# Performance work log

Measured on AMD Instinct MI355X. Metric: run time of the kernel, lower is better.

The kernel has to match this reference:

```python
import jax, jax.numpy as jnp
import numpy as np

RANK = 24          # init: rank
WHITEN = True      # init: whiten
NS_ITERS = 5       # Newton-Schulz iterations for inverse matrix square root
EPS = 1e-5         # covariance jitter


def _ns_inv_sqrt(C, iters=NS_ITERS):
    # Newton-Schulz iteration computing C^{-1/2} for SPD C: (B, N, N).
    N = C.shape[-1]
    I = jnp.eye(N, dtype=C.dtype)
    normC = jnp.sqrt(jnp.sum(C * C, axis=(-2, -1), keepdims=True))  # Frobenius norm
    Y = C / normC
    Z = jnp.broadcast_to(I, C.shape)
    for _ in range(iters):
        T = 0.5 * (3.0 * I - Z @ Y)
        Y = Y @ T
        Z = T @ Z
    return Z / jnp.sqrt(normC)  # Z -> norm^{1/2} * C^{-1/2}


def _whiten(X):
    # X: (B, n, N) -> X @ Cov(X)^{-1/2}
    n = X.shape[-2]
    N = X.shape[-1]
    C = jnp.einsum('bnd,bne->bde', X, X) / n + EPS * jnp.eye(N, dtype=X.dtype)
    return X @ _ns_inv_sqrt(C)


def _procrustes_rotation(M):
    # M = S^T T (B, d, d); orthogonal R = U Vh minimizing ||S R - T||_F (Kabsch).
    U, _, Vh = jnp.linalg.svd(M, full_matrices=False)
    return U @ Vh


def _align(source, target, rank=RANK, whiten=WHITEN):
    S = _whiten(source) if whiten else source
    T = _whiten(target) if whiten else target
    N = S.shape[-1]
    if N <= 32:
        # full Procrustes
        R = _procrustes_rotation(jnp.einsum('bnd,bne->bde', S, T))
        aligned = S @ R
    else:
        # project to rank-r joint subspace, align there, lift back with
        # identity on the orthogonal complement: R = Q Rr Q^T + (I - Q Q^T)
        X = jnp.concatenate([S, T], axis=1)                 # (B, 2n, N)
        _, _, Vh = jnp.linalg.svd(X, full_matrices=False)    # Vh: (B, N', N)
        Q = jnp.swapaxes(Vh[:, :rank, :], -2, -1)            # (B, N, r)
        Sp = S @ Q                                           # (B, n, r)
        Tp = T @ Q
        Rr = _procrustes_rotation(jnp.einsum('bnr,bns->brs', Sp, Tp))  # (B, r, r) small SVD
        # aligned = S @ (Q Rr Q^T + I - Q Q^T) = S + Sp (Rr - I) Q^T
        aligned = S + Sp @ (Rr - jnp.eye(rank, dtype=S.dtype)) @ jnp.swapaxes(Q, -2, -1)
    return aligned


def setup_inputs() -> dict:
    key = jax.random.key(0)
    k1, k2 = jax.random.split(key)
    source = jax.random.normal(k1, (64, 512, 384), dtype=jnp.float32)
    target = jax.random.normal(k2, (64, 512, 384), dtype=jnp.float32)
    return {"source": source, "target": target}


def reference(source, target):
    aligned = _align(source, target)
    # diagnostic: mean cosine similarity between aligned and target rows
    cos = jnp.sum(aligned * target, axis=-1) / (
        jnp.linalg.norm(aligned, axis=-1) * jnp.linalg.norm(target, axis=-1) + 1e-8)
    cos_after = jnp.mean(cos)
    return aligned, cos_after
```

## Files before the change

### kernel.cpp

```cpp
#include <hip/hip_runtime.h>
#include <math.h>

static constexpr int BATCH = 64;
static constexpr int NR  = 512;
static constexpr int ND  = 384;
static constexpr int RK  = 24;
static constexpr int NSI = 5;
static constexpr int POLAR_ITERS = 36;
static constexpr int PNB = 32;
static constexpr long SZC = (long)BATCH * ND * ND;
static constexpr int SSTR = BATCH * RK;

#define MODE_PLAIN 0
#define MODE_COV   1
#define MODE_NST   2
#define MODE_SCALE 3
#define MODE_ACC   4

typedef _Float16 half8 __attribute__((ext_vector_type(8)));
typedef _Float16 half4 __attribute__((ext_vector_type(4)));
typedef float floatx4 __attribute__((ext_vector_type(4)));

template<int TA>
__global__ __launch_bounds__(256)
void gemm_kernel(const float* __restrict__ Ag, const float* __restrict__ Bg,
                 float* __restrict__ Cg, int M, int N, int K,
                 long sA, long sB, long sC, int lda, int ldb, int ldc,
                 int mode, const float* __restrict__ scale)
{
    const int batch = blockIdx.y;
    const int tilesN = N >> 7;
    const int tx = blockIdx.x % tilesN;
    const int ty = blockIdx.x / tilesN;
    const int n0 = tx * 128, m0 = ty * 128;
    const float* A = Ag + (long)batch * sA;
    const float* Bm = Bg + (long)batch * sB;
    float* C = Cg + (long)batch * sC;

    __shared__ _Float16 Ah[128][40], Al[128][40];
    __shared__ _Float16 Bh[128][40], Bl[128][40];

    const int tid = threadIdx.x;
    const int wave = tid >> 6, lane = tid & 63;
    const int wm0 = (wave >> 1) * 64, wn0 = (wave & 1) * 64;
    const int fm = lane & 15;
    const int fq = lane >> 4;

    floatx4 acc[4][4];
#pragma unroll
    for (int i = 0; i < 4; i++)
#pragma unroll
        for (int j = 0; j < 4; j++) acc[i][j] = (floatx4){0.f, 0.f, 0.f, 0.f};

    for (int k0 = 0; k0 < K; k0 += 32) {
        if (TA == 0) {
#pragma unroll
            for (int q = 0; q < 4; q++) {
                int idx = tid + q * 256;
                int row = idx >> 3, kq = (idx & 7) * 4;
                float4 v = *(const float4*)&A[(long)(m0 + row) * lda + k0 + kq];
                _Float16 h0 = (_Float16)v.x; _Float16 l0 = (_Float16)(v.x - (float)h0);
                _Float16 h1 = (_Float16)v.y; _Float16 l1 = (_Float16)(v.y - (float)h1);
                _Float16 h2 = (_Float16)v.z; _Float16 l2 = (_Float16)(v.z - (float)h2);
                _Float16 h3 = (_Float16)v.w; _Float16 l3 = (_Float16)(v.w - (float)h3);
                half4 hv, lv;
                hv[0] = h0; hv[1] = h1; hv[2] = h2; hv[3] = h3;
                lv[0] = l0; lv[1] = l1; lv[2] = l2; lv[3] = l3;
                *(half4*)&Ah[row][kq] = hv;
                *(half4*)&Al[row][kq] = lv;
            }
        } else {
            int m = tid & 127, kb = (tid >> 7) * 16;
            _Float16 hbuf[16], lbuf[16];
#pragma unroll
            for (int i = 0; i < 16; i++) {
                float v = A[(long)(k0 + kb + i) * lda + m0 + m];
                _Float16 hh = (_Float16)v;
                hbuf[i] = hh; lbuf[i] = (_Float16)(v - (float)hh);
            }
#pragma unroll
            for (int i = 0; i < 16; i += 4) {
                half4 hv, lv;
                hv[0] = hbuf[i]; hv[1] = hbuf[i + 1]; hv[2] = hbuf[i + 2]; hv[3] = hbuf[i + 3];
                lv[0] = lbuf[i]; lv[1] = lbuf[i + 1]; lv[2] = lbuf[i + 2]; lv[3] = lbuf[i + 3];
                *(half4*)&Ah[m][kb + i] = hv;
                *(half4*)&Al[m][kb + i] = lv;
            }
        }
        {
            int n = tid & 127, kb = (tid >> 7) * 16;
            _Float16 hbuf[16], lbuf[16];
#pragma unroll
            for (int i = 0; i < 16; i++) {
                float v = Bm[(long)(k0 + kb + i) * ldb + n0 + n];
                _Float16 hh = (_Float16)v;
                hbuf[i] = hh; lbuf[i] = (_Float16)(v - (float)hh);
            }
#pragma unroll
            for (int i = 0; i < 16; i += 4) {
                half4 hv, lv;
                hv[0] = hbuf[i]; hv[1] = hbuf[i + 1]; hv[2] = hbuf[i + 2]; hv[3] = hbuf[i + 3];
                lv[0] = lbuf[i]; lv[1] = lbuf[i + 1]; lv[2] = lbuf[i + 2]; lv[3] = lbuf[i + 3];
                *(half4*)&Bh[n][kb + i] = hv;
                *(half4*)&Bl[n][kb + i] = lv;
            }
        }
        __syncthreads();

        half8 ah[4], alv[4], bh[4], blv[4];
#pragma unroll
        for (int mt = 0; mt < 4; mt++) {
            ah[mt]  = *(const half8*)&Ah[wm0 + mt * 16 + fm][fq * 8];
            alv[mt] = *(const half8*)&Al[wm0 + mt * 16 + fm][fq * 8];
        }
#pragma unroll
        for (int nt = 0; nt < 4; nt++) {
            bh[nt]  = *(const half8*)&Bh[wn0 + nt * 16 + fm][fq * 8];
            blv[nt] = *(const half8*)&Bl[wn0 + nt * 16 + fm][fq * 8];
        }
#pragma unroll
        for (int mt = 0; mt < 4; mt++) {
#pragma unroll
            for (int nt = 0; nt < 4; nt++) {
                floatx4 a = acc[mt][nt];
                a = __builtin_amdgcn_mfma_f32_16x16x32_f16(alv[mt], bh[nt], a, 0, 0, 0);
                a = __builtin_amdgcn_mfma_f32_16x16x32_f16(ah[mt], blv[nt], a, 0, 0, 0);
                a = __builtin_amdgcn_mfma_f32_16x16x32_f16(ah[mt], bh[nt], a, 0, 0, 0);
                acc[mt][nt] = a;
            }
        }
        __syncthreads();
    }

    float scl = 1.f;
    if (mode == MODE_SCALE) scl = 1.0f / sqrtf(scale[batch]);

#pragma unroll
    for (int mt = 0; mt < 4; mt++) {
#pragma unroll
        for (int nt = 0; nt < 4; nt++) {
            int gn = n0 + wn0 + nt * 16 + fm;
#pragma unroll
            for (int r = 0; r < 4; r++) {
                int gm = m0 + wm0 + mt * 16 + fq * 4 + r;
                float v = acc[mt][nt][r];
                float* cp = C + (long)gm * ldc + gn;
                if (mode == MODE_COV)      v = v * (1.0f / 512.0f) + ((gm == gn) ? 1e-5f : 0.f);
                else if (mode == MODE_NST) v = ((gm == gn) ? 1.5f : 0.f) - 0.5f * v;
                else if (mode == MODE_SCALE) v *= scl;
                else if (mode == MODE_ACC) v += *cp;
                *cp = v;
            }
        }
    }
}

__global__ __launch_bounds__(256)
void frob_kernel(const float* __restrict__ Cm, float* __restrict__ nrm)
{
    int b = blockIdx.x;
    const float* p = Cm + (long)b * ND * ND;
    float s = 0.f;
    for (int i = threadIdx.x; i < ND * ND; i += 256) { float v = p[i]; s += v * v; }
    __shared__ float red[256];
    red[threadIdx.x] = s; __syncthreads();
    for (int off = 128; off > 0; off >>= 1) {
        if (threadIdx.x < off) red[threadIdx.x] += red[threadIdx.x + off];
        __syncthreads();
    }
    if (threadIdx.x == 0) nrm[b] = sqrtf(red[0]);
}

__global__ __launch_bounds__(256)
void init_kernel(float* __restrict__ Y, float* __restrict__ Z, const float* __restrict__ nrm)
{
    const int total = BATCH * ND * ND;
    for (int idx = blockIdx.x * 256 + threadIdx.x; idx < total; idx += gridDim.x * 256) {
        int b = idx / (ND * ND);
        int rem = idx - b * (ND * ND);
        int r = rem / ND, c = rem - r * ND;
        Y[idx] = Y[idx] / nrm[b];
        Z[idx] = (r == c) ? 1.f : 0.f;
    }
}

__device__ __forceinline__ float bred768(float v, float* red12, int t)
{
#pragma unroll
    for (int off = 32; off > 0; off >>= 1) v += __shfl_down(v, off);
    if ((t & 63) == 0) red12[t >> 6] = v;
    __syncthreads();
    float r = 0.f;
#pragma unroll
    for (int i = 0; i < 12; i++) r += red12[i];
    __syncthreads();
    return r;
}

__global__ __launch_bounds__(768)
void tridiag_panel(float* __restrict__ Gall, float* __restrict__ dA,
                   float* __restrict__ eA, float* __restrict__ tauA,
                   float* __restrict__ Wgall, int k0)
{
    int b = blockIdx.x;
    float* A = Gall + (long)b * ND * ND;
    float* Wg = Wgall + (long)b * (PNB * ND);
    float* d = dA + b * ND; float* e = eA + b * ND; float* tau = tauA + b * ND;
    const int t = threadIdx.x;
    const int h = (t >= ND) ? 1 : 0;
    const int c = t - h * ND;
    const int g = t % 96;
    const int s = t / 96;
    __shared__ float Ul[PNB][ND];
    __shared__ float Wl[PNB][ND];
    __shared__ float u_s[ND];
    __shared__ float pp4s[8][392];
    __shared__ float al[PNB], be[PNB];
    __shared__ float red12[12];
    __shared__ float s_tau;

    const int jcnt = min(PNB, ND - 2 - k0);

    for (int j = 0; j < jcnt; j++) {
        const int k = k0 + j;
        const int m = ND - 1 - k;
        float x = 0.f;
        if (!h && c < m) {
            const int kc = (k + 1) + c;
            x = A[(long)k * ND + kc];
#pragma unroll 4
            for (int l = 0; l < j; l++) {
                x -= Ul[l][k] * Wl[l][kc] + Wl[l][k] * Ul[l][kc];
            }
            u_s[c] = x;
        }
        float sigma = bred768(x * x, red12, t);
        if (t == 0) {
            float v0 = u_s[0];
            float normx = sqrtf(sigma);
            float alpha = (v0 >= 0.f) ? -normx : normx;
            float denom = sigma - alpha * v0;
            float tk = (denom > 1e-30f) ? 1.f / denom : 0.f;
            s_tau = tk;
            float diag = A[(long)k * ND + k];
            for (int l = 0; l < j; l++) diag -= 2.f * Ul[l][k] * Wl[l][k];
            e[k] = alpha; tau[k] = tk; d[k] = diag;
            u_s[0] = v0 - alpha;
        }
        __syncthreads();
        const float tk = s_tau;

        const int kk4 = (k + 1) & ~3;
        const int off = (k + 1) - kk4;
        const int ncol4 = 96 - (kk4 >> 2);
        if (g < ncol4) {
            const int ri0 = (m * s) >> 3;
            const int ri1 = (m * (s + 1)) >> 3;
            const float* base = A + (long)(k + 1) * ND + kk4 + 4 * g;
            floatx4 p4 = (floatx4){0.f, 0.f, 0.f, 0.f};
            int i = ri0;
            for (; i + 8 <= ri1; i += 8) {
                floatx4 a0 = *(const floatx4*)&base[(long)(i    ) * ND];
                floatx4 a1 = *(const floatx4*)&base[(long)(i + 1) * ND];
                floatx4 a2 = *(const floatx4*)&base[(long)(i + 2) * ND];
                floatx4 a3 = *(const floatx4*)&base[(long)(i + 3) * ND];
                floatx4 a4 = *(const floatx4*)&base[(long)(i + 4) * ND];
                floatx4 a5 = *(const floatx4*)&base[(long)(i + 5) * ND];
                floatx4 a6 = *(const floatx4*)&base[(long)(i + 6) * ND];
                floatx4 a7 = *(const floatx4*)&base[(long)(i + 7) * ND];
                p4 += a0 * u_s[i]     + a1 * u_s[i + 1] + a2 * u_s[i + 2] + a3 * u_s[i + 3]
                    + a4 * u_s[i + 4] + a5 * u_s[i + 5] + a6 * u_s[i + 6] + a7 * u_s[i + 7];
            }
            for (; i < ri1; i++) {
                floatx4 a0 = *(const floatx4*)&base[(long)i * ND];
                p4 += a0 * u_s[i];
            }
            *(floatx4*)&pp4s[s][4 * g] = p4;
        }
        {
            int wv = t >> 6, ln = t & 63;
            for (int l = wv; l < j; l += 12) {
                float sa = 0.f, sb = 0.f;
                const float* wrow = &Wl[l][k + 1];
                const float* urow = &Ul[l][k + 1];
                for (int i = ln; i < m; i += 64) { sa += wrow[i] * u_s[i]; sb += urow[i] * u_s[i]; }
#pragma unroll
                for (int off2 = 32; off2 > 0; off2 >>= 1) {
                    sa += __shfl_down(sa, off2); sb += __shfl_down(sb, off2);
                }
                if (ln == 0) { al[l] = sa; be[l] = sb; }
            }
        }
        __syncthreads();
        float contrib = 0.f, pc = 0.f;
        if (!h && c < m) {
            int ca = c + off;
            pc = pp4s[0][ca] + pp4s[1][ca] + pp4s[2][ca] + pp4s[3][ca]
               + pp4s[4][ca] + pp4s[5][ca] + pp4s[6][ca] + pp4s[7][ca];
            const int kc = (k + 1) + c;
#pragma unroll 4
            for (int l = 0; l < j; l++) {
                pc -= al[l] * Ul[l][kc] + be[l] * Wl[l][kc];
            }
            pc *= tk;
            contrib = u_s[c] * pc;
        }
        float dotup = bred768(contrib, red12, t);
        float sc = 0.5f * tk * dotup;
        if (!h && c < m) {
            const int kc = (k + 1) + c;
            float uv = u_s[c];
            float w = pc - sc * uv;
            Wl[j][kc] = w;
            Ul[j][kc] = uv;
            Wg[j * ND + kc] = w;
            A[(long)k * ND + kc] = uv;
        }
        __syncthreads();
    }
    if (k0 + PNB >= ND - 2 && t == 0) {
        float d0 = A[(long)(ND - 2) * ND + (ND - 2)];
        float e0 = A[(long)(ND - 2) * ND + (ND - 1)];
        float d1 = A[(long)(ND - 1) * ND + (ND - 1)];
        for (int l = 0; l < jcnt; l++) {
            float u0 = A[(long)(k0 + l) * ND + (ND - 2)];
            float u1 = A[(long)(k0 + l) * ND + (ND - 1)];
            float w0 = Wg[l * ND + (ND - 2)];
            float w1 = Wg[l * ND + (ND - 1)];
            d0 -= 2.f * u0 * w0;
            e0 -= u0 * w1 + w0 * u1;
            d1 -= 2.f * u1 * w1;
        }
        d[ND - 2] = d0; d[ND - 1] = d1; e[ND - 2] = e0;
        e[ND - 1] = 0.f; tau[ND - 2] = 0.f; tau[ND - 1] = 0.f;
    }
}

__global__ __launch_bounds__(256)
void syr2k_update(float* __restrict__ Gall, const float* __restrict__ Wgall, int k0)
{
    const int k1 = k0 + PNB;
    const int tiles = (ND - k1) >> 5;
    int b = blockIdx.y;
    int ti = blockIdx.x / tiles, tj = blockIdx.x % tiles;
    int i0 = k1 + ti * 32, c0 = k1 + tj * 32;
    float* A = Gall + (long)b * ND * ND;
    const float* Wg = Wgall + (long)b * (PNB * ND);

    __shared__ float Us[PNB][36], Ws[PNB][36], Uc[PNB][36], Wc[PNB][36];
    int t = threadIdx.x;
    for (int q = t; q < PNB * 8; q += 256) {
        int l = q >> 3, c4 = (q & 7) * 4;
        *(float4*)&Us[l][c4] = *(const float4*)&A[(long)(k0 + l) * ND + i0 + c4];
        *(float4*)&Ws[l][c4] = *(const float4*)&Wg[l * ND + i0 + c4];
        *(float4*)&Uc[l][c4] = *(const float4*)&A[(long)(k0 + l) * ND + c0 + c4];
        *(float4*)&Wc[l][c4] = *(const float4*)&Wg[l * ND + c0 + c4];
    }
    __syncthreads();
    int tr = t >> 4, tc = t & 15;
    float acc00 = 0.f, acc01 = 0.f, acc10 = 0.f, acc11 = 0.f;
#pragma unroll 4
    for (int l = 0; l < PNB; l++) {
        float ua0 = Us[l][tr * 2], ua1 = Us[l][tr * 2 + 1];
        float wa0 = Ws[l][tr * 2], wa1 = Ws[l][tr * 2 + 1];
        float ub0 = Uc[l][tc * 2], ub1 = Uc[l][tc * 2 + 1];
        float wb0 = Wc[l][tc * 2], wb1 = Wc[l][tc * 2 + 1];
        acc00 += ua0 * wb0 + wa0 * ub0;
        acc01 += ua0 * wb1 + wa0 * ub1;
        acc10 += ua1 * wb0 + wa1 * ub0;
        acc11 += ua1 * wb1 + wa1 * ub1;
    }
    {
        float* r0 = &A[(long)(i0 + tr * 2) * ND + c0 + tc * 2];
        float* r1 = r0 + ND;
        float2 o0 = *(const float2*)r0, o1 = *(const float2*)r1;
        o0.x -= acc00; o0.y -= acc01;
        o1.x -= acc10; o1.y -= acc11;
        *(float2*)r0 = o0; *(float2*)r1 = o1;
    }
}

__global__ __launch_bounds__(64)
void eigvals_kernel(const float* __restrict__ dA, const float* __restrict__ eA,
                    float* __restrict__ lamA)
{
    int b = blockIdx.x, t = threadIdx.x;
    __shared__ float2 de[ND];
    __shared__ float d_s[ND], ea[ND], red[64];
    for (int i = t; i < ND; i += 64) {
        float dv = dA[b * ND + i];
        float ev = eA[b * ND + i];
        float ep = (i > 0) ? eA[b * ND + i - 1] : 0.f;
        d_s[i] = dv; ea[i] = fabsf(ev);
        de[i] = make_float2(dv, ep * ep + 1e-38f);
    }
    __syncthreads();
    float lo = 1e30f, hi = -1e30f;
    for (int i = t; i < ND; i += 64) {
        float r = ea[i] + ((i > 0) ? ea[i - 1] : 0.f);
        lo = fminf(lo, d_s[i] - r); hi = fmaxf(hi, d_s[i] + r);
    }
    red[t] = lo; __syncthreads();
    for (int off = 32; off > 0; off >>= 1) {
        if (t < off) red[t] = fminf(red[t], red[t + off]);
        __syncthreads();
    }
    lo = red[0]; __syncthreads();
    red[t] = hi; __syncthreads();
    for (int off = 32; off > 0; off >>= 1) {
        if (t < off) red[t] = fmaxf(red[t], red[t + off]);
        __syncthreads();
    }
    hi = red[0];
    if (t < RK) {
        int idx = ND - 1 - t;
        float a = lo, c = hi;
        for (int it = 0; it < 42; it++) {
            float mid = 0.5f * (a + c);
            int cnt = 0;
            float qinv = 0.f;
            for (int i = 0; i < ND; i += 8) {
                float2 v0 = de[i    ], v1 = de[i + 1], v2 = de[i + 2], v3 = de[i + 3];
                float2 v4 = de[i + 4], v5 = de[i + 5], v6 = de[i + 6], v7 = de[i + 7];
                float q;
                q = (v0.x - mid) - v0.y * qinv; cnt += (q < 0.f); qinv = __builtin_amdgcn_rcpf(q);
                q = (v1.x - mid) - v1.y * qinv; cnt += (q < 0.f); qinv = __builtin_amdgcn_rcpf(q);
                q = (v2.x - mid) - v2.y * qinv; cnt += (q < 0.f); qinv = __builtin_amdgcn_rcpf(q);
                q = (v3.x - mid) - v3.y * qinv; cnt += (q < 0.f); qinv = __builtin_amdgcn_rcpf(q);
                q = (v4.x - mid) - v4.y * qinv; cnt += (q < 0.f); qinv = __builtin_amdgcn_rcpf(q);
                q = (v5.x - mid) - v5.y * qinv; cnt += (q < 0.f); qinv = __builtin_amdgcn_rcpf(q);
                q = (v6.x - mid) - v6.y * qinv; cnt += (q < 0.f); qinv = __builtin_amdgcn_rcpf(q);
                q = (v7.x - mid) - v7.y * qinv; cnt += (q < 0.f); qinv = __builtin_amdgcn_rcpf(q);
            }
            if (cnt > idx) c = mid; else a = mid;
        }
        lamA[b * RK + t] = 0.5f * (a + c);
    }
}

__global__ __launch_bounds__(64)
void invit_kernel(const float* __restrict__ dA, const float* __restrict__ eA,
                  const float* __restrict__ lamA, float* __restrict__ scr)
{
    int b = blockIdx.x, t = threadIdx.x;
    __shared__ float d[ND], e[ND];
    __shared__ float ua[ND][RK], ub[ND][RK], uc[ND][RK];
    __shared__ float y[ND][RK];
    for (int i = t; i < ND; i += 64) { d[i] = dA[b * ND + i]; e[i] = eA[b * ND + i]; }
    __syncthreads();
    if (t >= RK) return;
    const int s = b * RK + t;
    float* yout = scr + 5L * ND * SSTR;
    const float lam = lamA[s];

    for (int pass = 0; pass < 2; pass++) {
        if (pass == 0) {
            for (int i = 0; i < ND; i++) {
                unsigned h = ((unsigned)i * 1103515245u) ^ ((unsigned)s * 747796405u);
                h *= 2654435769u; h ^= h >> 16;
                y[i][t] = ((float)(h & 0xFFFFu) * (1.f / 65536.f)) - 0.5f;
            }
        }
        float ai = d[0] - lam;
        float bc = e[0];
        float ycur = y[0][t];
        for (int i = 0; i < ND - 1; i++) {
            float sub = e[i];
            float dn = d[i + 1] - lam;
            float en = (i + 1 < ND - 1) ? e[i + 1] : 0.f;
            float ynext = y[i + 1][t];
            if (fabsf(ai) >= fabsf(sub)) {
                float aa = (ai == 0.f) ? 1e-20f : ai;
                float mlt = sub / aa;
                ua[i][t] = aa; ub[i][t] = bc; uc[i][t] = 0.f;
                y[i][t] = ycur;
                ycur = ynext - mlt * ycur;
                ai = dn - mlt * bc;
                bc = en;
            } else {
                float mlt = ai / sub;
                ua[i][t] = sub; ub[i][t] = dn; uc[i][t] = en;
                y[i][t] = ynext;
                ycur = ycur - mlt * ynext;
                ai = bc - mlt * dn;
                bc = -mlt * en;
            }
        }
        float uaN = (ai == 0.f) ? 1e-20f : ai;
        float x1 = ycur / uaN;
        y[ND - 1][t] = x1;
        float x2 = x1;
        {
            float xm = (y[ND - 2][t] - ub[ND - 2][t] * x1) / ua[ND - 2][t];
            y[ND - 2][t] = xm; x2 = x1; x1 = xm;
        }
        for (int i = ND - 3; i >= 0; i--) {
            float xi = (y[i][t] - ub[i][t] * x1 - uc[i][t] * x2) / ua[i][t];
            y[i][t] = xi; x2 = x1; x1 = xi;
        }
        float nn = 0.f;
        for (int i = 0; i < ND; i++) { float v = y[i][t]; nn += v * v; }
        float inv = (nn > 0.f) ? 1.f / sqrtf(nn) : 0.f;
        for (int i = 0; i < ND; i++) y[i][t] *= inv;
    }
    for (int i = 0; i < ND; i++) yout[(long)i * SSTR + s] = y[i][t];
}

__global__ __launch_bounds__(384)
void orthbt_kernel(const float* __restrict__ xx, const float* __restrict__ Gall,
                   const float* __restrict__ tauA, float* __restrict__ Qout)
{
    int b = blockIdx.x, t = threadIdx.x;
    __shared__ float Y[ND][RK + 1];
    __shared__ float red[ND];
    __shared__ float dts[RK];
    __shared__ float tls[ND];

    for (int j = 0; j < RK; j++) Y[t][j] = xx[(long)t * SSTR + b * RK + j];
    tls[t] = tauA[b * ND + t];
    __syncthreads();

    const int mcol = t % RK;
    const int msl  = t / RK;
    const int r0m  = msl * 24;
    for (int j = 0; j < RK; j++) {
        float pp = 0.f;
        for (int i = 0; i < 24; i++) {
            pp += Y[r0m + i][j] * Y[r0m + i][mcol];
        }
        red[mcol * 16 + msl] = pp;
        __syncthreads();
        if (t < RK) {
            float ssum = 0.f;
            for (int q = 0; q < 16; q++) ssum += red[t * 16 + q];
            dts[t] = ssum;
        }
        __syncthreads();
        float nv = dts[j];
        float inv = (nv > 1e-30f) ? (1.f / sqrtf(nv)) : 0.f;
        if (mcol > j) {
            float coef = dts[mcol] * inv * inv;
            for (int i = 0; i < 24; i++) Y[r0m + i][mcol] -= coef * Y[r0m + i][j];
        } else if (mcol == j) {
            for (int i = 0; i < 24; i++) Y[r0m + i][j] *= inv;
        }
        __syncthreads();
    }

    const int wv = t >> 6, ln = t & 63;
    float yr[4][6];
#pragma unroll
    for (int cc = 0; cc < 4; cc++)
#pragma unroll
        for (int q = 0; q < 6; q++)
            yr[cc][q] = Y[ln + 64 * q][4 * wv + cc];
    __syncthreads();

    const float* A = Gall + (long)b * ND * ND;
    float un[6];
    {
        const int k = ND - 3;
#pragma unroll
        for (int q = 0; q < 6; q++) un[q] = A[(long)k * ND + ln + 64 * q];
    }
    for (int k = ND - 3; k >= 0; k--) {
        float cu[6];
#pragma unroll
        for (int q = 0; q < 6; q++) {
            int r = ln + 64 * q;
            cu[q] = (r > k) ? un[q] : 0.f;
        }
        if (k > 0) {
#pragma unroll
            for (int q = 0; q < 6; q++) un[q] = A[(long)(k - 1) * ND + ln + 64 * q];
        }
        const float tk = tls[k];
#pragma unroll
        for (int cc = 0; cc < 4; cc++) {
            float p = 0.f;
#pragma unroll
            for (int q = 0; q < 6; q++) p += cu[q] * yr[cc][q];
#pragma unroll
            for (int off = 32; off > 0; off >>= 1) p += __shfl_xor(p, off);
            float sv = tk * p;
#pragma unroll
            for (int q = 0; q < 6; q++) yr[cc][q] -= sv * cu[q];
        }
    }

#pragma unroll
    for (int cc = 0; cc < 4; cc++)
#pragma unroll
        for (int q = 0; q < 6; q++)
            Y[ln + 64 * q][4 * wv + cc] = yr[cc][q];
    __syncthreads();
    for (int l = t; l < ND * RK; l += 384) {
        int i = l / RK, j = l - i * RK;
        Qout[(long)b * ND * RK + l] = Y[i][j];
    }
}

__global__ __launch_bounds__(256)
void proj_kernel(const float* __restrict__ Xw, const float* __restrict__ Qall,
                 float* __restrict__ P)
{
    int b = blockIdx.y;
    int r0 = blockIdx.x * 256;
    __shared__ float Qs[ND][RK + 1];
    const float* Q = Qall + (long)b * ND * RK;
    for (int l = threadIdx.x; l < ND * RK; l += 256) {
        int i = l / RK, j = l - i * RK;
        Qs[i][j] = Q[l];
    }
    __syncthreads();
    int r = r0 + threadIdx.x;
    const float* X = Xw + (long)b * NR * ND + (long)r * ND;
    float acc[RK];
#pragma unroll
    for (int j = 0; j < RK; j++) acc[j] = 0.f;
    for (int k = 0; k < ND; k++) {
        float xv = X[k];
#pragma unroll
        for (int j = 0; j < RK; j++) acc[j] += xv * Qs[k][j];
    }
    float* Pr = P + (long)b * NR * RK + (long)r * RK;
#pragma unroll
    for (int j = 0; j < RK; j++) Pr[j] = acc[j];
}

__global__ __launch_bounds__(256)
void polar_kernel(const float* __restrict__ Sp, const float* __restrict__ Tp,
                  float* __restrict__ RmI)
{
    int b = blockIdx.x, t = threadIdx.x;
    __shared__ float Sb[128][RK + 1], Tb[128][RK + 1];
    __shared__ float Xm[RK][RK + 1], Bm[RK][RK + 1], Mm[RK][RK + 1];
    __shared__ float red[256];

    float accM[3] = {0.f, 0.f, 0.f};
    for (int c = 0; c < 4; c++) {
        for (int l = t; l < 128 * RK; l += 256) {
            int row = l / RK, colj = l - row * RK;
            Sb[row][colj] = Sp[(long)b * NR * RK + (long)(c * 128 + row) * RK + colj];
            Tb[row][colj] = Tp[(long)b * NR * RK + (long)(c * 128 + row) * RK + colj];
        }
        __syncthreads();
        for (int q = 0; q < 3; q++) {
            int e = t + q * 256;
            if (e < RK * RK) {
                int r = e / RK, s2 = e - r * RK;
                float a = 0.f;
                for (int n = 0; n < 128; n++) a += Sb[n][r] * Tb[n][s2];
                accM[q] += a;
            }
        }
        __syncthreads();
    }
    float ss = 0.f;
    for (int q = 0; q < 3; q++) {
        int e = t + q * 256;
        if (e < RK * RK) {
            int r = e / RK, s2 = e - r * RK;
            Mm[r][s2] = accM[q];
            ss += accM[q] * accM[q];
        }
    }
    red[t] = ss; __syncthreads();
    for (int off = 128; off > 0; off >>= 1) {
        if (t < off) red[t] += red[t + off];
        __syncthreads();
    }
    float fro = sqrtf(red[0]);
    float inv = (fro > 1e-30f) ? 1.f / fro : 0.f;
    for (int q = 0; q < 3; q++) {
        int e = t + q * 256;
        if (e < RK * RK) { int r = e / RK, s2 = e - r * RK; Xm[r][s2] = Mm[r][s2] * inv; }
    }
    __syncthreads();
    for (int it = 0; it < POLAR_ITERS; it++) {
        for (int q = 0; q < 3; q++) {
            int e = t + q * 256;
            if (e < RK * RK) {
                int r = e / RK, s2 = e - r * RK;
                float a = 0.f;
                for (int k = 0; k < RK; k++) a += Xm[k][r] * Xm[k][s2];
                Bm[r][s2] = a;
            }
        }
        __syncthreads();
        for (int q = 0; q < 3; q++) {
            int e = t + q * 256;
            if (e < RK * RK) {
                int r = e / RK, s2 = e - r * RK;
                float a = 0.f;
                for (int k = 0; k < RK; k++) a += Xm[r][k] * Bm[k][s2];
                Mm[r][s2] = 1.5f * Xm[r][s2] - 0.5f * a;
            }
        }
        __syncthreads();
        for (int q = 0; q < 3; q++) {
            int e = t + q * 256;
            if (e < RK * RK) { int r = e / RK, s2 = e - r * RK; Xm[r][s2] = Mm[r][s2]; }
        }
        __syncthreads();
    }
    for (int q = 0; q < 3; q++) {
        int e = t + q * 256;
        if (e < RK * RK) {
            int r = e / RK, s2 = e - r * RK;
            RmI[(long)b * RK * RK + e] = Xm[r][s2] - ((r == s2) ? 1.f : 0.f);
        }
    }
}

__global__ __launch_bounds__(256)
void align_kernel(const float* __restrict__ Sw, const float* __restrict__ Sp,
                  const float* __restrict__ RmI, const float* __restrict__ Qall,
                  float* __restrict__ out)
{
    int b = blockIdx.y;
    int r0 = blockIdx.x * 64;
    int t = threadIdx.x;
    __shared__ float Qs[ND][RK + 1];
    __shared__ float Rm[RK][RK + 1];
    __shared__ float Ss[64][RK + 1];
    __shared__ float W[64][RK + 1];

    for (int l = t; l < ND * RK; l += 256) {
        int i = l / RK, j = l - i * RK;
        Qs[i][j] = Qall[(long)b * ND * RK + l];
    }
    for (int l = t; l < RK * RK; l += 256) {
        int i = l / RK, j = l - i * RK;
        Rm[i][j] = RmI[(long)b * RK * RK + l];
    }
    for (int l = t; l < 64 * RK; l += 256) {
        int i = l / RK, j = l - i * RK;
        Ss[i][j] = Sp[(long)b * NR * RK + (long)(r0 + i) * RK + j];
    }
    __syncthreads();
    for (int l = t; l < 64 * RK; l += 256) {
        int r = l / RK, j = l - r * RK;
        float a = 0.f;
        for (int k = 0; k < RK; k++) a += Ss[r][k] * Rm[k][j];
        W[r][j] = a;
    }
    __syncthreads();
    for (int r = 0; r < 64; r++) {
        for (int c = t; c < ND; c += 256) {
            float a = Sw[(long)b * NR * ND + (long)(r0 + r) * ND + c];
            float s2 = 0.f;
#pragma unroll
            for (int j = 0; j < RK; j++) s2 += W[r][j] * Qs[c][j];
            out[(long)b * NR * ND + (long)(r0 + r) * ND + c] = a + s2;
        }
    }
}

__global__ __launch_bounds__(256)
void cos_kernel(const float* __restrict__ out, const float* __restrict__ tgt,
                float* __restrict__ acc)
{
    int row = blockIdx.x * 4 + (threadIdx.x >> 6);
    int lane = threadIdx.x & 63;
    const float* a = out + (long)row * ND;
    const float* tg = tgt + (long)row * ND;
    float sd = 0.f, sa = 0.f, st = 0.f;
    for (int i = lane; i < ND; i += 64) {
        float av = a[i], tv = tg[i];
        sd += av * tv; sa += av * av; st += tv * tv;
    }
#pragma unroll
    for (int off = 32; off > 0; off >>= 1) {
        sd += __shfl_down(sd, off); sa += __shfl_down(sa, off); st += __shfl_down(st, off);
    }
    __shared__ float part[4];
    if (lane == 0) part[threadIdx.x >> 6] = sd / (sqrtf(sa) * sqrtf(st) + 1e-8f);
    __syncthreads();
    if (threadIdx.x == 0) atomicAdd(acc, part[0] + part[1] + part[2] + part[3]);
}

__global__ void finalize_kernel(const float* __restrict__ acc, float* __restrict__ out)
{
    out[0] = acc[0] / 32768.0f;
}

static inline void launch_gemm(int TA, const float* A, const float* Bm, float* C,
                               int M, int N, int K, long sA, long sB, long sC,
                               int lda, int ldb, int ldc, int mode,
                               const float* scale, hipStream_t stream)
{
    dim3 grid((M / 128) * (N / 128), BATCH);
    if (TA)
        gemm_kernel<1><<<grid, dim3(256), 0, stream>>>(A, Bm, C, M, N, K, sA, sB, sC, lda, ldb, ldc, mode, scale);
    else
        gemm_kernel<0><<<grid, dim3(256), 0, stream>>>(A, Bm, C, M, N, K, sA, sB, sC, lda, ldb, ldc, mode, scale);
}

extern "C" void kernel_launch(void* const* d_in, const int* in_sizes, int n_in,
                              void* d_out, int out_size, void* d_ws, size_t ws_size,
                              hipStream_t stream)
{
    const float* src = (const float*)d_in[0];
    const float* tgt = (const float*)d_in[1];
    float* out = (float*)d_out;
    float* ws = (float*)d_ws;

    float* A0 = ws;
    float* A1 = ws + 1 * SZC;
    float* A2 = ws + 2 * SZC;
    float* A3 = ws + 3 * SZC;
    float* A4 = ws + 4 * SZC;
    float* S5 = ws + 5 * SZC;
    float* nrm_s = S5;
    float* nrm_t = S5 + 64;
    float* dd = S5 + 128;
    float* ee = dd + BATCH * ND;
    float* tt = ee + BATCH * ND;
    float* lam = tt + BATCH * ND;
    float* accp = lam + BATCH * RK;

    float* Tm = out;
    float* SW = A0;
    float* TW = A0 + (long)BATCH * NR * ND;
    float* G  = A3;
    float* scr = A4;
    float* Qp  = A4 + 6L * ND * SSTR;
    float* Spp = Qp + (long)BATCH * ND * RK;
    float* Tpp = Spp + (long)BATCH * NR * RK;
    float* Rp  = Tpp + (long)BATCH * NR * RK;
    float* Wg  = Rp + (long)BATCH * RK * RK;
    float* yarr = scr + 5L * ND * SSTR;

    const long sXin = (long)NR * ND;
    const long sSq  = (long)ND * ND;

    launch_gemm(1, src, src, A0, ND, ND, NR, sXin, sXin, sSq, ND, ND, ND, MODE_COV, nullptr, stream);
    frob_kernel<<<BATCH, 256, 0, stream>>>(A0, nrm_s);
    init_kernel<<<dim3(4096), 256, 0, stream>>>(A0, A2, nrm_s);
    {
        float* Y = A0; float* Yo = A1; float* Z = A2; float* Zo = A3;
        for (int it = 0; it < NSI; it++) {
            launch_gemm(0, Z, Y, Tm, ND, ND, ND, sSq, sSq, sSq, ND, ND, ND, MODE_NST, nullptr, stream);
            launch_gemm(0, Y, Tm, Yo, ND, ND, ND, sSq, sSq, sSq, ND, ND, ND, MODE_PLAIN, nullptr, stream);
            launch_gemm(0, Tm, Z, Zo, ND, ND, ND, sSq, sSq, sSq, ND, ND, ND, MODE_PLAIN, nullptr, stream);
            float* tmp = Y; Y = Yo; Yo = tmp;
            tmp = Z; Z = Zo; Zo = tmp;
        }
    }
    launch_gemm(1, tgt, tgt, A0, ND, ND, NR, sXin, sXin, sSq, ND, ND, ND, MODE_COV, nullptr, stream);
    frob_kernel<<<BATCH, 256, 0, stream>>>(A0, nrm_t);
    init_kernel<<<dim3(4096), 256, 0, stream>>>(A0, A2, nrm_t);
    {
        float* Y = A0; float* Yo = A1; float* Z = A2; float* Zo = A4;
        for (int it = 0; it < NSI; it++) {
            launch_gemm(0, Z, Y, Tm, ND, ND, ND, sSq, sSq, sSq, ND, ND, ND, MODE_NST, nullptr, stream);
            launch_gemm(0, Y, Tm, Yo, ND, ND, ND, sSq, sSq, sSq, ND, ND, ND, MODE_PLAIN, nullptr, stream);
            launch_gemm(0, Tm, Z, Zo, ND, ND, ND, sSq, sSq, sSq, ND, ND, ND, MODE_PLAIN, nullptr, stream);
            float* tmp = Y; Y = Yo; Yo = tmp;
            tmp = Z; Z = Zo; Zo = tmp;
        }
    }
    launch_gemm(0, src, A3, SW, NR, ND, ND, sXin, sSq, sXin, ND, ND, ND, MODE_SCALE, nrm_s, stream);
    launch_gemm(0, tgt, A4, TW, NR, ND, ND, sXin, sSq, sXin, ND, ND, ND, MODE_SCALE, nrm_t, stream);
    launch_gemm(1, SW, SW, G, ND, ND, NR, sXin, sXin, sSq, ND, ND, ND, MODE_PLAIN, nullptr, stream);
    launch_gemm(1, TW, TW, G, ND, ND, NR, sXin, sXin, sSq, ND, ND, ND, MODE_ACC, nullptr, stream);
    for (int p = 0; p < ND / PNB; p++) {
        tridiag_panel<<<BATCH, 768, 0, stream>>>(G, dd, ee, tt, Wg, p * PNB);
        int k1 = (p + 1) * PNB;
        if (k1 < ND - 2) {
            int tiles = (ND - k1) >> 5;
            syr2k_update<<<dim3(tiles * tiles, BATCH), 256, 0, stream>>>(G, Wg, p * PNB);
        }
    }
    eigvals_kernel<<<BATCH, 64, 0, stream>>>(dd, ee, lam);
    invit_kernel<<<BATCH, 64, 0, stream>>>(dd, ee, lam, scr);
    orthbt_kernel<<<BATCH, 384, 0, stream>>>(yarr, G, tt, Qp);
    proj_kernel<<<dim3(2, BATCH), 256, 0, stream>>>(SW, Qp, Spp);
    proj_kernel<<<dim3(2, BATCH), 256, 0, stream>>>(TW, Qp, Tpp);
    polar_kernel<<<BATCH, 256, 0, stream>>>(Spp, Tpp, Rp);
    align_kernel<<<dim3(8, BATCH), 256, 0, stream>>>(SW, Spp, Rp, Qp, out);
    hipMemsetAsync((void*)accp, 0, 4, stream);
    cos_kernel<<<dim3(8192), 256, 0, stream>>>(out, tgt, accp);
    finalize_kernel<<<1, 1, 0, stream>>>(accp, out + (long)BATCH * NR * ND);
    (void)in_sizes; (void)n_in; (void)out_size; (void)ws_size;
}
```

Baseline: 5.774 ms.

## Exploit symmetry in Newton-Schulz and covariance GEMMs and fuse the T construction

The Newton-Schulz iteration is reformulated so that every iterate is a symmetric polynomial in the normalized covariance. The separate T = 1.5I - 0.5ZY GEMM output mode is replaced by applying that affine map on the fly while the A/B operand tiles are loaded (tmask). A symmetric mode computes only the upper-triangular 128x128 tiles and mirrors them with transposed stores, and it is applied to the covariance, Gram and NS GEMMs. The aim is to cut MFMA work and tile count by roughly a third. In exchange the mirrored writes are uncoalesced, and the reordered iteration relies on commutativity, which holds only up to floating-point error.

```diff
diff --git a/kernel.cpp b/kernel.cpp
--- a/kernel.cpp
+++ b/kernel.cpp
@@ -5,7 +5,6 @@
 static constexpr int NR  = 512;
 static constexpr int ND  = 384;
 static constexpr int RK  = 24;
-static constexpr int NSI = 5;
 static constexpr int POLAR_ITERS = 36;
 static constexpr int PNB = 32;
 static constexpr long SZC = (long)BATCH * ND * ND;
@@ -13,7 +12,6 @@
 
 #define MODE_PLAIN 0
 #define MODE_COV   1
-#define MODE_NST   2
 #define MODE_SCALE 3
 #define MODE_ACC   4
 
@@ -26,13 +24,21 @@
 void gemm_kernel(const float* __restrict__ Ag, const float* __restrict__ Bg,
                  float* __restrict__ Cg, int M, int N, int K,
                  long sA, long sB, long sC, int lda, int ldb, int ldc,
-                 int mode, const float* __restrict__ scale)
+                 int mode, const float* __restrict__ scale, int sym, int tmask)
 {
     const int batch = blockIdx.y;
     const int tilesN = N >> 7;
-    const int tx = blockIdx.x % tilesN;
-    const int ty = blockIdx.x / tilesN;
-    const int n0 = tx * 128, m0 = ty * 128;
+    int ti, tj;
+    if (sym) {
+        int idx = blockIdx.x;
+        ti = 0; int rem = tilesN;
+        while (idx >= rem) { idx -= rem; ti++; rem--; }
+        tj = ti + idx;
+    } else {
+        tj = blockIdx.x % tilesN;
+        ti = blockIdx.x / tilesN;
+    }
+    const int n0 = tj * 128, m0 = ti * 128;
     const float* A = Ag + (long)batch * sA;
     const float* Bm = Bg + (long)batch * sB;
     float* C = Cg + (long)batch * sC;
@@ -59,6 +65,13 @@
                 int idx = tid + q * 256;
                 int row = idx >> 3, kq = (idx & 7) * 4;
                 float4 v = *(const float4*)&A[(long)(m0 + row) * lda + k0 + kq];
+                if (tmask & 1) {
+                    int gr = m0 + row, gc = k0 + kq;
+                    v.x = ((gr == gc    ) ? 1.5f : 0.f) - 0.5f * v.x;
+                    v.y = ((gr == gc + 1) ? 1.5f : 0.f) - 0.5f * v.y;
+                    v.z = ((gr == gc + 2) ? 1.5f : 0.f) - 0.5f * v.z;
+                    v.w = ((gr == gc + 3) ? 1.5f : 0.f) - 0.5f * v.w;
+                }
                 _Float16 h0 = (_Float16)v.x; _Float16 l0 = (_Float16)(v.x - (float)h0);
                 _Float16 h1 = (_Float16)v.y; _Float16 l1 = (_Float16)(v.y - (float)h1);
                 _Float16 h2 = (_Float16)v.z; _Float16 l2 = (_Float16)(v.z - (float)h2);
@@ -93,6 +106,7 @@
 #pragma unroll
             for (int i = 0; i < 16; i++) {
                 float v = Bm[(long)(k0 + kb + i) * ldb + n0 + n];
+                if (tmask & 2) v = (((k0 + kb + i) == (n0 + n)) ? 1.5f : 0.f) - 0.5f * v;
                 _Float16 hh = (_Float16)v;
                 hbuf[i] = hh; lbuf[i] = (_Float16)(v - (float)hh);
             }
@@ -143,13 +157,19 @@
 #pragma unroll
             for (int r = 0; r < 4; r++) {
                 int gm = m0 + wm0 + mt * 16 + fq * 4 + r;
-                float v = acc[mt][nt][r];
+                float a = acc[mt][nt][r];
                 float* cp = C + (long)gm * ldc + gn;
-                if (mode == MODE_COV)      v = v * (1.0f / 512.0f) + ((gm == gn) ? 1e-5f : 0.f);
-                else if (mode == MODE_NST) v = ((gm == gn) ? 1.5f : 0.f) - 0.5f * v;
-                else if (mode == MODE_SCALE) v *= scl;
-                else if (mode == MODE_ACC) v += *cp;
+                float v = a;
+                if (mode == MODE_COV)      v = a * (1.0f / 512.0f) + ((gm == gn) ? 1e-5f : 0.f);
+                else if (mode == MODE_SCALE) v = a * scl;
+                else if (mode == MODE_ACC) v = a + *cp;
                 *cp = v;
+                if (sym && ti != tj) {
+                    float* cq = C + (long)gn * ldc + gm;
+                    float vq = v;
+                    if (mode == MODE_ACC) vq = a + *cq;
+                    *cq = vq;
+                }
             }
         }
     }
@@ -172,15 +192,16 @@
 }
 
 __global__ __launch_bounds__(256)
-void init_kernel(float* __restrict__ Y, float* __restrict__ Z, const float* __restrict__ nrm)
+void initns_kernel(float* __restrict__ Mb, float* __restrict__ Z, const float* __restrict__ nrm)
 {
     const int total = BATCH * ND * ND;
     for (int idx = blockIdx.x * 256 + threadIdx.x; idx < total; idx += gridDim.x * 256) {
         int b = idx / (ND * ND);
         int rem = idx - b * (ND * ND);
         int r = rem / ND, c = rem - r * ND;
-        Y[idx] = Y[idx] / nrm[b];
-        Z[idx] = (r == c) ? 1.f : 0.f;
+        float v = Mb[idx] / nrm[b];
+        Mb[idx] = v;
+        Z[idx] = ((r == c) ? 1.5f : 0.f) - 0.5f * v;
     }
 }
 
@@ -788,13 +809,16 @@
 static inline void launch_gemm(int TA, const float* A, const float* Bm, float* C,
                                int M, int N, int K, long sA, long sB, long sC,
                                int lda, int ldb, int ldc, int mode,
-                               const float* scale, hipStream_t stream)
-{
-    dim3 grid((M / 128) * (N / 128), BATCH);
+                               const float* scale, int sym, int tmask, hipStream_t stream)
+{
+    int tiles;
+    if (sym) { int tn = N >> 7; tiles = tn * (tn + 1) / 2; }
+    else tiles = (M / 128) * (N / 128);
+    dim3 grid(tiles, BATCH);
     if (TA)
-        gemm_kernel<1><<<grid, dim3(256), 0, stream>>>(A, Bm, C, M, N, K, sA, sB, sC, lda, ldb, ldc, mode, scale);
+        gemm_kernel<1><<<grid, dim3(256), 0, stream>>>(A, Bm, C, M, N, K, sA, sB, sC, lda, ldb, ldc, mode, scale, sym, tmask);
     else
-        gemm_kernel<0><<<grid, dim3(256), 0, stream>>>(A, Bm, C, M, N, K, sA, sB, sC, lda, ldb, ldc, mode, scale);
+        gemm_kernel<0><<<grid, dim3(256), 0, stream>>>(A, Bm, C, M, N, K, sA, sB, sC, lda, ldb, ldc, mode, scale, sym, tmask);
 }
 
 extern "C" void kernel_launch(void* const* d_in, const int* in_sizes, int n_in,
@@ -823,6 +847,7 @@
     float* Tm = out;
     float* SW = A0;
     float* TW = A0 + (long)BATCH * NR * ND;
+    float* B4 = TW;
     float* G  = A3;
     float* scr = A4;
     float* Qp  = A4 + 6L * ND * SSTR;
@@ -835,36 +860,42 @@
     const long sXin = (long)NR * ND;
     const long sSq  = (long)ND * ND;
 
-    launch_gemm(1, src, src, A0, ND, ND, NR, sXin, sXin, sSq, ND, ND, ND, MODE_COV, nullptr, stream);
-    frob_kernel<<<BATCH, 256, 0, stream>>>(A0, nrm_s);
-    init_kernel<<<dim3(4096), 256, 0, stream>>>(A0, A2, nrm_s);
-    {
-        float* Y = A0; float* Yo = A1; float* Z = A2; float* Zo = A3;
-        for (int it = 0; it < NSI; it++) {
-            launch_gemm(0, Z, Y, Tm, ND, ND, ND, sSq, sSq, sSq, ND, ND, ND, MODE_NST, nullptr, stream);
-            launch_gemm(0, Y, Tm, Yo, ND, ND, ND, sSq, sSq, sSq, ND, ND, ND, MODE_PLAIN, nullptr, stream);
-            launch_gemm(0, Tm, Z, Zo, ND, ND, ND, sSq, sSq, sSq, ND, ND, ND, MODE_PLAIN, nullptr, stream);
-            float* tmp = Y; Y = Yo; Yo = tmp;
-            tmp = Z; Z = Zo; Zo = tmp;
-        }
-    }
-    launch_gemm(1, tgt, tgt, A0, ND, ND, NR, sXin, sXin, sSq, ND, ND, ND, MODE_COV, nullptr, stream);
-    frob_kernel<<<BATCH, 256, 0, stream>>>(A0, nrm_t);
-    init_kernel<<<dim3(4096), 256, 0, stream>>>(A0, A2, nrm_t);
-    {
-        float* Y = A0; float* Yo = A1; float* Z = A2; float* Zo = A4;
-        for (int it = 0; it < NSI; it++) {
-            launch_gemm(0, Z, Y, Tm, ND, ND, ND, sSq, sSq, sSq, ND, ND, ND, MODE_NST, nullptr, stream);
-            launch_gemm(0, Y, Tm, Yo, ND, ND, ND, sSq, sSq, sSq, ND, ND, ND, MODE_PLAIN, nullptr, stream);
-            launch_gemm(0, Tm, Z, Zo, ND, ND, ND, sSq, sSq, sSq, ND, ND, ND, MODE_PLAIN, nullptr, stream);
-            float* tmp = Y; Y = Yo; Yo = tmp;
-            tmp = Z; Z = Zo; Zo = tmp;
-        }
-    }
-    launch_gemm(0, src, A3, SW, NR, ND, ND, sXin, sSq, sXin, ND, ND, ND, MODE_SCALE, nrm_s, stream);
-    launch_gemm(0, tgt, A4, TW, NR, ND, ND, sXin, sSq, sXin, ND, ND, ND, MODE_SCALE, nrm_t, stream);
-    launch_gemm(1, SW, SW, G, ND, ND, NR, sXin, sXin, sSq, ND, ND, ND, MODE_PLAIN, nullptr, stream);
-    launch_gemm(1, TW, TW, G, ND, ND, NR, sXin, sXin, sSq, ND, ND, ND, MODE_ACC, nullptr, stream);
+    launch_gemm(1, src, src, A3, ND, ND, NR, sXin, sXin, sSq, ND, ND, ND, MODE_COV, nullptr, 1, 0, stream);
+    frob_kernel<<<BATCH, 256, 0, stream>>>(A3, nrm_s);
+    initns_kernel<<<dim3(2048), 256, 0, stream>>>(A3, A4, nrm_s);
+    launch_gemm(0, A3, A3, Tm, ND, ND, ND, sSq, sSq, sSq, ND, ND, ND, MODE_PLAIN, nullptr, 1, 3, stream);
+    launch_gemm(0, A3, Tm, A0, ND, ND, ND, sSq, sSq, sSq, ND, ND, ND, MODE_PLAIN, nullptr, 1, 0, stream);
+    launch_gemm(0, A0, A4, A3, ND, ND, ND, sSq, sSq, sSq, ND, ND, ND, MODE_PLAIN, nullptr, 1, 1, stream);
+    launch_gemm(0, A0, A0, Tm, ND, ND, ND, sSq, sSq, sSq, ND, ND, ND, MODE_PLAIN, nullptr, 1, 3, stream);
+    launch_gemm(0, A0, Tm, A4, ND, ND, ND, sSq, sSq, sSq, ND, ND, ND, MODE_PLAIN, nullptr, 1, 0, stream);
+    launch_gemm(0, A4, A3, A0, ND, ND, ND, sSq, sSq, sSq, ND, ND, ND, MODE_PLAIN, nullptr, 1, 1, stream);
+    launch_gemm(0, A4, A4, Tm, ND, ND, ND, sSq, sSq, sSq, ND, ND, ND, MODE_PLAIN, nullptr, 1, 3, stream);
+    launch_gemm(0, A4, Tm, A3, ND, ND, ND, sSq, sSq, sSq, ND, ND, ND, MODE_PLAIN, nullptr, 1, 0, stream);
+    launch_gemm(0, A3, A0, A4, ND, ND, ND, sSq, sSq, sSq, ND, ND, ND, MODE_PLAIN, nullptr, 1, 1, stream);
+    launch_gemm(0, A3, A3, Tm, ND, ND, ND, sSq, sSq, sSq, ND, ND, ND, MODE_PLAIN, nullptr, 1, 3, stream);
+    launch_gemm(0, A3, Tm, A0, ND, ND, ND, sSq, sSq, sSq, ND, ND, ND, MODE_PLAIN, nullptr, 1, 0, stream);
+    launch_gemm(0, A0, A4, A3, ND, ND, ND, sSq, sSq, sSq, ND, ND, ND, MODE_PLAIN, nullptr, 1, 1, stream);
+    launch_gemm(0, src, A3, SW, NR, ND, ND, sXin, sSq, sXin, ND, ND, ND, MODE_SCALE, nrm_s, 0, 0, stream);
+
+    launch_gemm(1, tgt, tgt, A3, ND, ND, NR, sXin, sXin, sSq, ND, ND, ND, MODE_COV, nullptr, 1, 0, stream);
+    frob_kernel<<<BATCH, 256, 0, stream>>>(A3, nrm_t);
+    initns_kernel<<<dim3(2048), 256, 0, stream>>>(A3, A4, nrm_t);
+    launch_gemm(0, A3, A3, Tm, ND, ND, ND, sSq, sSq, sSq, ND, ND, ND, MODE_PLAIN, nullptr, 1, 3, stream);
+    launch_gemm(0, A3, Tm, B4, ND, ND, ND, sSq, sSq, sSq, ND, ND, ND, MODE_PLAIN, nullptr, 1, 0, stream);
+    launch_gemm(0, B4, A4, A3, ND, ND, ND, sSq, sSq, sSq, ND, ND, ND, MODE_PLAIN, nullptr, 1, 1, stream);
+    launch_gemm(0, B4, B4, Tm, ND, ND, ND, sSq, sSq, sSq, ND, ND, ND, MODE_PLAIN, nullptr, 1, 3, stream);
+    launch_gemm(0, B4, Tm, A4, ND, ND, ND, sSq, sSq, sSq, ND, ND, ND, MODE_PLAIN, nullptr, 1, 0, stream);
+    launch_gemm(0, A4, A3, B4, ND, ND, ND, sSq, sSq, sSq, ND, ND, ND, MODE_PLAIN, nullptr, 1, 1, stream);
+    launch_gemm(0, A4, A4, Tm, ND, ND, ND, sSq, sSq, sSq, ND, ND, ND, MODE_PLAIN, nullptr, 1, 3, stream);
+    launch_gemm(0, A4, Tm, A3, ND, ND, ND, sSq, sSq, sSq, ND, ND, ND, MODE_PLAIN, nullptr, 1, 0, stream);
+    launch_gemm(0, A3, B4, A4, ND, ND, ND, sSq, sSq, sSq, ND, ND, ND, MODE_PLAIN, nullptr, 1, 1, stream);
+    launch_gemm(0, A3, A3, Tm, ND, ND, ND, sSq, sSq, sSq, ND, ND, ND, MODE_PLAIN, nullptr, 1, 3, stream);
+    launch_gemm(0, A3, Tm, B4, ND, ND, ND, sSq, sSq, sSq, ND, ND, ND, MODE_PLAIN, nullptr, 1, 0, stream);
+    launch_gemm(0, B4, A4, A3, ND, ND, ND, sSq, sSq, sSq, ND, ND, ND, MODE_PLAIN, nullptr, 1, 1, stream);
+    launch_gemm(0, tgt, A3, TW, NR, ND, ND, sXin, sSq, sXin, ND, ND, ND, MODE_SCALE, nrm_t, 0, 0, stream);
+
+    launch_gemm(1, SW, SW, G, ND, ND, NR, sXin, sXin, sSq, ND, ND, ND, MODE_PLAIN, nullptr, 1, 0, stream);
+    launch_gemm(1, TW, TW, G, ND, ND, NR, sXin, sXin, sSq, ND, ND, ND, MODE_ACC, nullptr, 1, 0, stream);
     for (int p = 0; p < ND / PNB; p++) {
         tridiag_panel<<<BATCH, 768, 0, stream>>>(G, dd, ee, tt, Wg, p * PNB);
         int k1 = (p + 1) * PNB;
```

After: 5.640 ms. -2.3%, faster.
